# Kernel tuning notes

Measured on AMD Instinct MI355X. Metric: run time of the kernel, lower is better.

The kernel has to match this reference:

```python
import jax, jax.numpy as jnp
import numpy as np

INF = 1e10
B, T, D, N, H = 4, 1024, 1024, 16, 4096
SCALE = float(np.sqrt(D))  # Attention built with d_key = d_model in original code


def _linear(x, w, b):
    return x @ w.T + b


def _layernorm(x, gamma, beta, eps=1e-6):
    # torch x.std(-1) is unbiased (ddof=1); eps added to std, matching original
    m = x.mean(-1, keepdims=True)
    var = ((x - m) ** 2).sum(-1, keepdims=True) / (x.shape[-1] - 1)
    return gamma * (x - m) / (jnp.sqrt(var) + eps) + beta


def _mha(q_in, k_in, v_in, wq, bq, wk, bk, wv, bv, wo, bo, mask, causal):
    Bb, Tq, Dm = q_in.shape
    Tk = k_in.shape[1]
    dh = Dm // N
    q = _linear(q_in, wq, bq).reshape(Bb, Tq, N, dh).transpose(0, 2, 1, 3)  # b n q d
    k = _linear(k_in, wk, bk).reshape(Bb, Tk, N, dh).transpose(0, 2, 1, 3)
    v = _linear(v_in, wv, bv).reshape(Bb, Tk, N, dh).transpose(0, 2, 1, 3)
    dots = jnp.einsum('bnqd,bnkd->bnqk', q, k)
    if causal and Tq == Tk:
        tri = jnp.triu(jnp.ones((Tq, Tk), dots.dtype), 1) * INF
        dots = dots - tri
    dots = dots - (1.0 - mask)[:, None, None, :] * INF  # mask: 1=keep
    probs = jax.nn.softmax(dots / SCALE, axis=-1)
    out = jnp.einsum('bnqk,bnkd->bnqd', probs, v)
    out = out.transpose(0, 2, 1, 3).reshape(Bb, Tq, Dm)
    return _linear(out, wo, bo)


def setup_inputs() -> dict:
    key = jax.random.key(0)
    ks = jax.random.split(key, 16)
    g = lambda k, shp: (jax.random.normal(k, shp, dtype=jnp.float32) * 0.02)
    inp = {
        'x': jax.random.normal(ks[0], (B, T, D), dtype=jnp.float32),
        'encoding': jax.random.normal(ks[1], (B, T, D), dtype=jnp.float32),
        'mask_src': jnp.ones((B, T), dtype=jnp.float32),
        'mask_trg': jnp.ones((B, T), dtype=jnp.float32),
        # causal self-attention projections
        'sa_wq': g(ks[2], (D, D)), 'sa_bq': jnp.zeros((D,), jnp.float32),
        'sa_wk': g(ks[3], (D, D)), 'sa_bk': jnp.zeros((D,), jnp.float32),
        'sa_wv': g(ks[4], (D, D)), 'sa_bv': jnp.zeros((D,), jnp.float32),
        'sa_wo': g(ks[5], (D, D)), 'sa_bo': jnp.zeros((D,), jnp.float32),
        'sa_gamma': jnp.ones((D,), jnp.float32), 'sa_beta': jnp.zeros((D,), jnp.float32),
        # cross-attention projections
        'ca_wq': g(ks[6], (D, D)), 'ca_bq': jnp.zeros((D,), jnp.float32),
        'ca_wk': g(ks[7], (D, D)), 'ca_bk': jnp.zeros((D,), jnp.float32),
        'ca_wv': g(ks[8], (D, D)), 'ca_bv': jnp.zeros((D,), jnp.float32),
        'ca_wo': g(ks[9], (D, D)), 'ca_bo': jnp.zeros((D,), jnp.float32),
        'ca_gamma': jnp.ones((D,), jnp.float32), 'ca_beta': jnp.zeros((D,), jnp.float32),
        # feedforward
        'ff_w1': g(ks[10], (H, D)), 'ff_b1': jnp.zeros((H,), jnp.float32),
        'ff_w2': g(ks[11], (D, H)), 'ff_b2': jnp.zeros((D,), jnp.float32),
        'ff_gamma': jnp.ones((D,), jnp.float32), 'ff_beta': jnp.zeros((D,), jnp.float32),
    }
    return inp


def reference(x, encoding, mask_src, mask_trg,
              sa_wq, sa_bq, sa_wk, sa_bk, sa_wv, sa_bv, sa_wo, sa_bo, sa_gamma, sa_beta,
              ca_wq, ca_bq, ca_wk, ca_bk, ca_wv, ca_bv, ca_wo, ca_bo, ca_gamma, ca_beta,
              ff_w1, ff_b1, ff_w2, ff_b2, ff_gamma, ff_beta):
    # DecoderLayer forward (eval: dropout = identity)
    h = _layernorm(x + _mha(x, x, x, sa_wq, sa_bq, sa_wk, sa_bk, sa_wv, sa_bv,
                            sa_wo, sa_bo, mask_trg, causal=True), sa_gamma, sa_beta)
    h = _layernorm(h + _mha(h, encoding, encoding, ca_wq, ca_bq, ca_wk, ca_bk,
                            ca_wv, ca_bv, ca_wo, ca_bo, mask_src, causal=False),
                   ca_gamma, ca_beta)
    ff = _linear(jax.nn.relu(_linear(h, ff_w1, ff_b1)), ff_w2, ff_b2)
    return _layernorm(h + ff, ff_gamma, ff_beta)
```

## Files before the change

kernel.cpp:

```cpp
#include <hip/hip_runtime.h>
#include <hip/hip_bf16.h>
#include <math.h>
#include <stdint.h>

#define BATCH   4
#define TSEQ    1024
#define DMODEL  1024
#define NHEAD   16
#define DHEAD   64
#define HFF     4096
#define MROWS   (BATCH * TSEQ)

typedef _Float16 f16;
typedef __attribute__((ext_vector_type(2))) _Float16 f16x2;
typedef __attribute__((ext_vector_type(4))) _Float16 f16x4;
typedef __attribute__((ext_vector_type(8))) _Float16 f16x8;
typedef __attribute__((ext_vector_type(4))) float    f32x4;

__global__ __launch_bounds__(256)
void cvt_f32_f16(const float* __restrict__ in, f16* __restrict__ out, int n)
{
    const int i = (blockIdx.x * 256 + threadIdx.x) * 8;
    if (i < n) {
        const float4 a = *(const float4*)(in + i);
        const float4 b = *(const float4*)(in + i + 4);
        f16x8 o;
        o[0] = (_Float16)a.x; o[1] = (_Float16)a.y; o[2] = (_Float16)a.z; o[3] = (_Float16)a.w;
        o[4] = (_Float16)b.x; o[5] = (_Float16)b.y; o[6] = (_Float16)b.z; o[7] = (_Float16)b.w;
        *(f16x8*)(out + i) = o;
    }
}

template<int TN, bool RES, bool RELU>
__global__ __launch_bounds__(256, 2)
void hgemm(const f16* __restrict__ A, const f16* __restrict__ Wt,
           const float* __restrict__ bias, const f16* __restrict__ Rm,
           f16* __restrict__ C, int M, int N, int K)
{
    constexpr int TM = 128, TK = 32;
    constexpr int NB = TN / 32;
    constexpr int AISS = (TM * TK) / (256 * 8);
    constexpr int BISS = (TN * TK) / (256 * 8);
    __shared__ alignas(16) f16 As[2][TM * TK];
    __shared__ alignas(16) f16 Bs[2][TN * TK];

    const int t = threadIdx.x, ln = t & 63, wv = t >> 6;
    const int wr = wv >> 1, wc = wv & 1;
    const size_t m0 = (size_t)blockIdx.y * TM, n0 = (size_t)blockIdx.x * TN;

    f32x4 acc[4][NB];
#pragma unroll
    for (int i = 0; i < 4; ++i)
#pragma unroll
        for (int j = 0; j < NB; ++j) acc[i][j] = (f32x4){0.f, 0.f, 0.f, 0.f};

    const f16* Ag = A + (m0 + (t >> 2)) * (size_t)K + (t & 3) * 8;
    const f16* Bg = Wt + (n0 + (t >> 2)) * (size_t)K + (t & 3) * 8;

    auto stage = [&](int buf, int k0) {
#pragma unroll
        for (int i = 0; i < AISS; ++i)
            __builtin_amdgcn_global_load_lds(
                (const __attribute__((address_space(1))) unsigned int*)(Ag + (size_t)(i * 64) * K + k0),
                (__attribute__((address_space(3))) unsigned int*)(&As[buf][(i * 256 + wv * 64) * 8]),
                16, 0, 0);
#pragma unroll
        for (int i = 0; i < BISS; ++i)
            __builtin_amdgcn_global_load_lds(
                (const __attribute__((address_space(1))) unsigned int*)(Bg + (size_t)(i * 64) * K + k0),
                (__attribute__((address_space(3))) unsigned int*)(&Bs[buf][(i * 256 + wv * 64) * 8]),
                16, 0, 0);
    };

    stage(0, 0);
    __syncthreads();
    int buf = 0;
    for (int k0 = 0; k0 < K; k0 += TK) {
        if (k0 + TK < K) stage(buf ^ 1, k0 + TK);
        f16x8 af[4], bf[NB];
        const f16* Ab = As[buf];
        const f16* Bb = Bs[buf];
#pragma unroll
        for (int i = 0; i < 4; ++i)
            af[i] = *(const f16x8*)(Ab + (wr * 64 + i * 16 + (ln & 15)) * TK + (ln >> 4) * 8);
#pragma unroll
        for (int j = 0; j < NB; ++j)
            bf[j] = *(const f16x8*)(Bb + (wc * (TN / 2) + j * 16 + (ln & 15)) * TK + (ln >> 4) * 8);
#pragma unroll
        for (int i = 0; i < 4; ++i)
#pragma unroll
            for (int j = 0; j < NB; ++j)
                acc[i][j] = __builtin_amdgcn_mfma_f32_16x16x32_f16(af[i], bf[j], acc[i][j], 0, 0, 0);
        __syncthreads();
        buf ^= 1;
    }

    const int colbase = (int)n0 + wc * (TN / 2) + (ln & 15);
    const int rowbase = (int)m0 + wr * 64 + (ln >> 4) * 4;
#pragma unroll
    for (int i = 0; i < 4; ++i) {
#pragma unroll
        for (int j = 0; j < NB; ++j) {
            const int col = colbase + j * 16;
            const float bj = bias[col];
#pragma unroll
            for (int r = 0; r < 4; ++r) {
                const int row = rowbase + i * 16 + r;
                float v = acc[i][j][r] + bj;
                if (RES) v += (float)Rm[(size_t)row * N + col];
                if (RELU) v = fmaxf(v, 0.f);
                C[(size_t)row * N + col] = (f16)v;
            }
        }
    }
}

template<bool CAUSAL>
__global__ __launch_bounds__(256, 2)
void attn_mfma(const f16* __restrict__ Qp, int qstr,
               const f16* __restrict__ Kp, int kstr,
               const f16* __restrict__ Vp, int vstr,
               const float* __restrict__ maskp,
               f16* __restrict__ Op)
{
    __shared__ alignas(16) f16 Ks[64 * 64];
    __shared__ alignas(16) f16 Vt[64 * 64];
    __shared__ alignas(16) f16 Ps[4][16 * 64];
    __shared__ alignas(16) float Msk[64];

    const int t = threadIdx.x, l = t & 63, wv = t >> 6;
    const int g = l >> 4, lq = l & 15, a = l & 7;
    const int bh = blockIdx.y, b = bh >> 4, h = bh & 15;
    const int q0 = blockIdx.x * 64;
    const int q0w = q0 + wv * 16;
    const int bT = b * TSEQ;

    f16x8 qf[2];
    {
        const f16* qp = Qp + (size_t)(bT + q0w + lq) * qstr + h * 64 + g * 8;
        qf[0] = *(const f16x8*)(qp);
        qf[1] = *(const f16x8*)(qp + 32);
    }

    f32x4 oacc[4];
#pragma unroll
    for (int i = 0; i < 4; ++i) oacc[i] = (f32x4){0.f, 0.f, 0.f, 0.f};
    float mrun = -1e30f, lrun = 0.f;

    const float* mrow = maskp + b * TSEQ;
    const int kend = CAUSAL ? (q0 + 64) : TSEQ;
    const int qmaxw = q0w + 15;

    f16x8 kr0, kr1, vr0, vr1;
    float mreg = 0.f;
    const int kkey = t >> 3, kd8 = t & 7;

    auto issue_loads = [&](int k0) {
        kr0 = *(const f16x8*)(Kp + (size_t)(bT + k0 + kkey) * kstr + h * 64 + kd8 * 8);
        kr1 = *(const f16x8*)(Kp + (size_t)(bT + k0 + 32 + kkey) * kstr + h * 64 + kd8 * 8);
        vr0 = *(const f16x8*)(Vp + (size_t)(bT + k0 + l) * vstr + h * 64 + wv * 8);
        vr1 = *(const f16x8*)(Vp + (size_t)(bT + k0 + l) * vstr + h * 64 + (4 + wv) * 8);
        if (t < 64) mreg = mrow[k0 + t];
    };
    auto write_stage = [&]() {
        *(f16x8*)&Ks[kkey * 64 + ((kd8 * 8) ^ ((kkey & 7) * 8))] = kr0;
        const int k2 = kkey + 32;
        *(f16x8*)&Ks[k2 * 64 + ((kd8 * 8) ^ ((k2 & 7) * 8))] = kr1;
#pragma unroll
        for (int e = 0; e < 8; ++e) {
            const int d0 = wv * 8 + e;
            const int d1 = (4 + wv) * 8 + e;
            Vt[d0 * 64 + (l ^ (e * 8))] = vr0[e];
            Vt[d1 * 64 + (l ^ (e * 8))] = vr1[e];
        }
        if (t < 64) Msk[t] = mreg;
    };

    issue_loads(0);
    write_stage();
    __syncthreads();

    f16* Pw = Ps[wv];

    for (int k0 = 0; k0 < kend; k0 += 64) {
        const int knext = k0 + 64;
        if (knext < kend) issue_loads(knext);

        if (!CAUSAL || k0 <= qmaxw) {
            f32x4 sacc[4];
#pragma unroll
            for (int kt = 0; kt < 4; ++kt) {
                const int row = kt * 16 + lq;
                const int sw = (row & 7) * 8;
                const f16x8 a0 = *(const f16x8*)&Ks[row * 64 + ((g * 8) ^ sw)];
                const f16x8 a1 = *(const f16x8*)&Ks[row * 64 + (((4 + g) * 8) ^ sw)];
                f32x4 z = (f32x4){0.f, 0.f, 0.f, 0.f};
                z = __builtin_amdgcn_mfma_f32_16x16x32_f16(a0, qf[0], z, 0, 0, 0);
                sacc[kt] = __builtin_amdgcn_mfma_f32_16x16x32_f16(a1, qf[1], z, 0, 0, 0);
            }
            float p[4][4];
            float tmax = -3.0e38f;
#pragma unroll
            for (int kt = 0; kt < 4; ++kt) {
                const float4 mk = *(const float4*)&Msk[kt * 16 + g * 4];
                const float mka[4] = {mk.x, mk.y, mk.z, mk.w};
#pragma unroll
                for (int r = 0; r < 4; ++r) {
                    float s = sacc[kt][r] * (1.f / 32.f) - (1.f - mka[r]) * 3.125e8f;
                    if (CAUSAL) {
                        const int key = k0 + kt * 16 + g * 4 + r;
                        if (key > q0w + lq) s = -3.0e38f;
                    }
                    p[kt][r] = s;
                    tmax = fmaxf(tmax, s);
                }
            }
            tmax = fmaxf(tmax, __shfl_xor(tmax, 16));
            tmax = fmaxf(tmax, __shfl_xor(tmax, 32));
            const float mnew = fmaxf(mrun, tmax);
            const float corr = __expf(mrun - mnew);
            mrun = mnew;
            lrun *= corr;
#pragma unroll
            for (int i = 0; i < 4; ++i) {
                oacc[i][0] *= corr; oacc[i][1] *= corr;
                oacc[i][2] *= corr; oacc[i][3] *= corr;
            }
            float rsum = 0.f;
#pragma unroll
            for (int kt = 0; kt < 4; ++kt)
#pragma unroll
                for (int r = 0; r < 4; ++r) {
                    const float e = __expf(p[kt][r] - mnew);
                    p[kt][r] = e;
                    rsum += e;
                }
            rsum += __shfl_xor(rsum, 16);
            rsum += __shfl_xor(rsum, 32);
            lrun += rsum;
#pragma unroll
            for (int kt = 0; kt < 4; ++kt) {
                f16x4 pv;
                pv[0] = (_Float16)p[kt][0]; pv[1] = (_Float16)p[kt][1];
                pv[2] = (_Float16)p[kt][2]; pv[3] = (_Float16)p[kt][3];
                const int kb = kt * 16 + g * 4;
                *(f16x4*)&Pw[lq * 64 + (kb ^ (a * 8))] = pv;
            }
            const f16x8 pf0 = *(const f16x8*)&Pw[lq * 64 + ((g * 8) ^ (a * 8))];
            const f16x8 pf1 = *(const f16x8*)&Pw[lq * 64 + (((4 + g) * 8) ^ (a * 8))];
#pragma unroll
            for (int dt = 0; dt < 4; ++dt) {
                const int row = dt * 16 + lq;
                const int sw = (row & 7) * 8;
                const f16x8 v0 = *(const f16x8*)&Vt[row * 64 + ((g * 8) ^ sw)];
                const f16x8 v1 = *(const f16x8*)&Vt[row * 64 + (((4 + g) * 8) ^ sw)];
                oacc[dt] = __builtin_amdgcn_mfma_f32_16x16x32_f16(v0, pf0, oacc[dt], 0, 0, 0);
                oacc[dt] = __builtin_amdgcn_mfma_f32_16x16x32_f16(v1, pf1, oacc[dt], 0, 0, 0);
            }
        }

        __syncthreads();
        if (knext < kend) write_stage();
        __syncthreads();
    }

    const float inv = 1.f / lrun;
#pragma unroll
    for (int dt = 0; dt < 4; ++dt) {
        f16x4 ov;
        ov[0] = (_Float16)(oacc[dt][0] * inv); ov[1] = (_Float16)(oacc[dt][1] * inv);
        ov[2] = (_Float16)(oacc[dt][2] * inv); ov[3] = (_Float16)(oacc[dt][3] * inv);
        const int db = dt * 16 + g * 4;
        *(f16x4*)&Pw[lq * 64 + (db ^ (a * 8))] = ov;
    }
#pragma unroll
    for (int i = 0; i < 2; ++i) {
        const int c = i * 64 + l;
        const int row = c >> 3, c8 = c & 7;
        const f16x8 ov = *(const f16x8*)&Pw[row * 64 + ((c8 * 8) ^ ((row & 7) * 8))];
        *(f16x8*)(Op + (size_t)(bT + q0w + row) * DMODEL + h * 64 + c8 * 8) = ov;
    }
}

__inline__ __device__ float block_sum256(float v, float* sm)
{
#pragma unroll
    for (int off = 32; off > 0; off >>= 1) v += __shfl_down(v, off, 64);
    const int lane = threadIdx.x & 63, w = threadIdx.x >> 6;
    if (lane == 0) sm[w] = v;
    __syncthreads();
    const float r = sm[0] + sm[1] + sm[2] + sm[3];
    __syncthreads();
    return r;
}

template<bool F32OUT>
__global__ __launch_bounds__(256)
void ln_kernel(const f16* __restrict__ X, const float* __restrict__ g,
               const float* __restrict__ be, void* __restrict__ Yv)
{
    __shared__ float sm[4];
    const int row = blockIdx.x;
    const size_t base = (size_t)row * DMODEL + threadIdx.x * 4;
    const f16x4 xv = *(const f16x4*)(X + base);
    float x[4] = {(float)xv[0], (float)xv[1], (float)xv[2], (float)xv[3]};

    float s = x[0] + x[1] + x[2] + x[3];
    s = block_sum256(s, sm);
    const float mean = s * (1.0f / (float)DMODEL);

    float dx[4] = {x[0] - mean, x[1] - mean, x[2] - mean, x[3] - mean};
    float s2 = dx[0] * dx[0] + dx[1] * dx[1] + dx[2] * dx[2] + dx[3] * dx[3];
    s2 = block_sum256(s2, sm);
    const float rs = 1.0f / (sqrtf(s2 * (1.0f / (float)(DMODEL - 1))) + 1e-6f);

    const float4 gv = *(const float4*)(g + threadIdx.x * 4);
    const float4 bv = *(const float4*)(be + threadIdx.x * 4);
    const float y0 = gv.x * dx[0] * rs + bv.x;
    const float y1 = gv.y * dx[1] * rs + bv.y;
    const float y2 = gv.z * dx[2] * rs + bv.z;
    const float y3 = gv.w * dx[3] * rs + bv.w;
    if (F32OUT) {
        float4 y = {y0, y1, y2, y3};
        *(float4*)((float*)Yv + base) = y;
    } else {
        f16x4 y; y[0] = (_Float16)y0; y[1] = (_Float16)y1; y[2] = (_Float16)y2; y[3] = (_Float16)y3;
        *(f16x4*)((f16*)Yv + base) = y;
    }
}

extern "C" void kernel_launch(void* const* d_in, const int* in_sizes, int n_in,
                              void* d_out, int out_size, void* d_ws, size_t ws_size,
                              hipStream_t stream)
{
    (void)in_sizes; (void)n_in; (void)out_size; (void)ws_size;

    const float* x        = (const float*)d_in[0];
    const float* enc      = (const float*)d_in[1];
    const float* mask_src = (const float*)d_in[2];
    const float* mask_trg = (const float*)d_in[3];
    const float* sa_wq = (const float*)d_in[4];  const float* sa_bq = (const float*)d_in[5];
    const float* sa_wk = (const float*)d_in[6];  const float* sa_bk = (const float*)d_in[7];
    const float* sa_wv = (const float*)d_in[8];  const float* sa_bv = (const float*)d_in[9];
    const float* sa_wo = (const float*)d_in[10]; const float* sa_bo = (const float*)d_in[11];
    const float* sa_g  = (const float*)d_in[12]; const float* sa_b  = (const float*)d_in[13];
    const float* ca_wq = (const float*)d_in[14]; const float* ca_bq = (const float*)d_in[15];
    const float* ca_wk = (const float*)d_in[16]; const float* ca_bk = (const float*)d_in[17];
    const float* ca_wv = (const float*)d_in[18]; const float* ca_bv = (const float*)d_in[19];
    const float* ca_wo = (const float*)d_in[20]; const float* ca_bo = (const float*)d_in[21];
    const float* ca_g  = (const float*)d_in[22]; const float* ca_b  = (const float*)d_in[23];
    const float* ff_w1 = (const float*)d_in[24]; const float* ff_b1 = (const float*)d_in[25];
    const float* ff_w2 = (const float*)d_in[26]; const float* ff_b2 = (const float*)d_in[27];
    const float* ff_g  = (const float*)d_in[28]; const float* ff_b  = (const float*)d_in[29];

    f16* ws = (f16*)d_ws;
    const size_t MEG = 1024 * 1024;
    f16* Wh = ws;
    f16* G  = ws + 4 * MEG;
    f16* S0 = ws + 20 * MEG;
    f16* S1 = ws + 24 * MEG;
    f16* S2 = ws + 28 * MEG;
    f16* S3 = ws + 32 * MEG;
    f16* S4 = ws + 36 * MEG;
    f16* S5 = ws + 40 * MEG;
    float* Bias = (float*)((char*)d_ws + 88 * MEG);

    const int NACT = MROWS * DMODEL;
    const int NW   = DMODEL * DMODEL;

    dim3 blk(256);
    const int cvAct = NACT / 2048, cvW = NW / 2048, cvFF = (4 * NW) / 2048;
    dim3 gQKV(3072 / 128, MROWS / 128);
    dim3 gN64(DMODEL / 64, MROWS / 128);
    dim3 gKV(2048 / 128, MROWS / 128);
    dim3 gFF1(HFF / 128, MROWS / 128);
    dim3 agrid(TSEQ / 64, BATCH * NHEAD);

    cvt_f32_f16<<<cvAct, blk, 0, stream>>>(x, S0, NACT);
    cvt_f32_f16<<<cvAct, blk, 0, stream>>>(enc, S1, NACT);
    cvt_f32_f16<<<cvW, blk, 0, stream>>>(sa_wq, Wh, NW);
    cvt_f32_f16<<<cvW, blk, 0, stream>>>(sa_wk, Wh + 1 * MEG, NW);
    cvt_f32_f16<<<cvW, blk, 0, stream>>>(sa_wv, Wh + 2 * MEG, NW);
    hipMemcpyAsync(Bias + 0,    sa_bq, 4096, hipMemcpyDeviceToDevice, stream);
    hipMemcpyAsync(Bias + 1024, sa_bk, 4096, hipMemcpyDeviceToDevice, stream);
    hipMemcpyAsync(Bias + 2048, sa_bv, 4096, hipMemcpyDeviceToDevice, stream);
    hgemm<128, false, false><<<gQKV, blk, 0, stream>>>(S0, Wh, Bias, nullptr, G, MROWS, 3072, DMODEL);
    attn_mfma<true><<<agrid, blk, 0, stream>>>(G, 3072, G + 1024, 3072, G + 2048, 3072, mask_trg, S2);
    cvt_f32_f16<<<cvW, blk, 0, stream>>>(sa_wo, Wh, NW);
    hipMemcpyAsync(Bias, sa_bo, 4096, hipMemcpyDeviceToDevice, stream);
    hgemm<64, true, false><<<gN64, blk, 0, stream>>>(S2, Wh, Bias, S0, S3, MROWS, DMODEL, DMODEL);
    ln_kernel<false><<<MROWS, blk, 0, stream>>>(S3, sa_g, sa_b, S4);

    cvt_f32_f16<<<cvW, blk, 0, stream>>>(ca_wq, Wh, NW);
    hipMemcpyAsync(Bias, ca_bq, 4096, hipMemcpyDeviceToDevice, stream);
    hgemm<64, false, false><<<gN64, blk, 0, stream>>>(S4, Wh, Bias, nullptr, G, MROWS, DMODEL, DMODEL);
    cvt_f32_f16<<<cvW, blk, 0, stream>>>(ca_wk, Wh, NW);
    cvt_f32_f16<<<cvW, blk, 0, stream>>>(ca_wv, Wh + 1 * MEG, NW);
    hipMemcpyAsync(Bias + 0,    ca_bk, 4096, hipMemcpyDeviceToDevice, stream);
    hipMemcpyAsync(Bias + 1024, ca_bv, 4096, hipMemcpyDeviceToDevice, stream);
    hgemm<128, false, false><<<gKV, blk, 0, stream>>>(S1, Wh, Bias, nullptr, G + 4 * MEG, MROWS, 2048, DMODEL);
    attn_mfma<false><<<agrid, blk, 0, stream>>>(G, 1024, G + 4 * MEG, 2048, G + 4 * MEG + 1024, 2048, mask_src, S2);
    cvt_f32_f16<<<cvW, blk, 0, stream>>>(ca_wo, Wh, NW);
    hipMemcpyAsync(Bias, ca_bo, 4096, hipMemcpyDeviceToDevice, stream);
    hgemm<64, true, false><<<gN64, blk, 0, stream>>>(S2, Wh, Bias, S4, S3, MROWS, DMODEL, DMODEL);
    ln_kernel<false><<<MROWS, blk, 0, stream>>>(S3, ca_g, ca_b, S5);

    cvt_f32_f16<<<cvFF, blk, 0, stream>>>(ff_w1, Wh, 4 * NW);
    hipMemcpyAsync(Bias, ff_b1, 16384, hipMemcpyDeviceToDevice, stream);
    hgemm<128, false, true><<<gFF1, blk, 0, stream>>>(S5, Wh, Bias, nullptr, G, MROWS, HFF, DMODEL);
    cvt_f32_f16<<<cvFF, blk, 0, stream>>>(ff_w2, Wh, 4 * NW);
    hipMemcpyAsync(Bias, ff_b2, 4096, hipMemcpyDeviceToDevice, stream);
    hgemm<64, true, false><<<gN64, blk, 0, stream>>>(G, Wh, Bias, S5, S3, MROWS, DMODEL, HFF);
    ln_kernel<true><<<MROWS, blk, 0, stream>>>(S3, ff_g, ff_b, d_out);
}
```

Before: 574.4 us.

## Fuse fp32 weight conversion into GEMM B-loads and swizzle block order

The GEMM now reads fp32 weights straight from the original buffers, converts them to fp16 in registers and writes them to LDS. This removes the separate weight-conversion kernels and the bias memcpys, and bias is indexed per 1024-column segment. It also fixes the N tile at 128 for every GEMM and adds an 8-way block-index swizzle meant to improve cache locality. In exchange, each GEMM reads twice the weight bytes per tile, the B path goes through registers instead of the direct global-to-LDS load, and the N=1024 GEMMs launch fewer blocks.

```diff
diff --git a/kernel.cpp b/kernel.cpp
--- a/kernel.cpp
+++ b/kernel.cpp
@@ -31,22 +31,37 @@
     }
 }
 
-template<int TN, bool RES, bool RELU>
+template<bool RES, bool RELU>
 __global__ __launch_bounds__(256, 2)
-void hgemm(const f16* __restrict__ A, const f16* __restrict__ Wt,
-           const float* __restrict__ bias, const f16* __restrict__ Rm,
-           f16* __restrict__ C, int M, int N, int K)
-{
-    constexpr int TM = 128, TK = 32;
-    constexpr int NB = TN / 32;
-    constexpr int AISS = (TM * TK) / (256 * 8);
-    constexpr int BISS = (TN * TK) / (256 * 8);
+void hgemm(const f16* __restrict__ A,
+           const float* __restrict__ w0, const float* __restrict__ w1,
+           const float* __restrict__ w2, const float* __restrict__ w3,
+           const float* __restrict__ b0, const float* __restrict__ b1,
+           const float* __restrict__ b2, const float* __restrict__ b3,
+           const f16* __restrict__ Rm, f16* __restrict__ C,
+           int M, int N, int K)
+{
+    constexpr int TM = 128, TN = 128, TK = 32;
+    constexpr int NB = 4;
+    constexpr int AISS = 2;
+    constexpr int BISS = 2;
     __shared__ alignas(16) f16 As[2][TM * TK];
     __shared__ alignas(16) f16 Bs[2][TN * TK];
 
     const int t = threadIdx.x, ln = t & 63, wv = t >> 6;
     const int wr = wv >> 1, wc = wv & 1;
-    const size_t m0 = (size_t)blockIdx.y * TM, n0 = (size_t)blockIdx.x * TN;
+
+    const int gx = gridDim.x, nb = gx * gridDim.y;
+    const int d  = blockIdx.y * gx + blockIdx.x;
+    const int wid = (d & 7) * (nb >> 3) + (d >> 3);
+    const int bx = wid % gx, by = wid / gx;
+
+    const size_t m0 = (size_t)by * TM, n0 = (size_t)bx * TN;
+
+    const float* wseg[4] = {w0, w1, w2, w3};
+    const float* bseg[4] = {b0, b1, b2, b3};
+    const float* Wg = wseg[n0 >> 10] + ((n0 & 1023) + (t >> 2)) * (size_t)K + (t & 3) * 8;
+    const f16*   Ag = A + (m0 + (t >> 2)) * (size_t)K + (t & 3) * 8;
 
     f32x4 acc[4][NB];
 #pragma unroll
@@ -54,29 +69,45 @@
 #pragma unroll
         for (int j = 0; j < NB; ++j) acc[i][j] = (f32x4){0.f, 0.f, 0.f, 0.f};
 
-    const f16* Ag = A + (m0 + (t >> 2)) * (size_t)K + (t & 3) * 8;
-    const f16* Bg = Wt + (n0 + (t >> 2)) * (size_t)K + (t & 3) * 8;
-
-    auto stage = [&](int buf, int k0) {
+    auto stage_A = [&](int buf, int k0) {
 #pragma unroll
         for (int i = 0; i < AISS; ++i)
             __builtin_amdgcn_global_load_lds(
                 (const __attribute__((address_space(1))) unsigned int*)(Ag + (size_t)(i * 64) * K + k0),
                 (__attribute__((address_space(3))) unsigned int*)(&As[buf][(i * 256 + wv * 64) * 8]),
                 16, 0, 0);
-#pragma unroll
-        for (int i = 0; i < BISS; ++i)
-            __builtin_amdgcn_global_load_lds(
-                (const __attribute__((address_space(1))) unsigned int*)(Bg + (size_t)(i * 64) * K + k0),
-                (__attribute__((address_space(3))) unsigned int*)(&Bs[buf][(i * 256 + wv * 64) * 8]),
-                16, 0, 0);
     };
 
-    stage(0, 0);
+    float4 br[BISS][2];
+    auto issue_B = [&](int k0) {
+#pragma unroll
+        for (int i = 0; i < BISS; ++i) {
+            br[i][0] = *(const float4*)(Wg + (size_t)(i * 64) * K + k0);
+            br[i][1] = *(const float4*)(Wg + (size_t)(i * 64) * K + k0 + 4);
+        }
+    };
+    auto write_B = [&](int buf) {
+#pragma unroll
+        for (int i = 0; i < BISS; ++i) {
+            f16x8 v;
+            v[0] = (_Float16)br[i][0].x; v[1] = (_Float16)br[i][0].y;
+            v[2] = (_Float16)br[i][0].z; v[3] = (_Float16)br[i][0].w;
+            v[4] = (_Float16)br[i][1].x; v[5] = (_Float16)br[i][1].y;
+            v[6] = (_Float16)br[i][1].z; v[7] = (_Float16)br[i][1].w;
+            *(f16x8*)&Bs[buf][(i * 256 + t) * 8] = v;
+        }
+    };
+
+    stage_A(0, 0);
+    issue_B(0);
+    write_B(0);
     __syncthreads();
+
     int buf = 0;
     for (int k0 = 0; k0 < K; k0 += TK) {
-        if (k0 + TK < K) stage(buf ^ 1, k0 + TK);
+        const int knext = k0 + TK;
+        if (knext < K) { stage_A(buf ^ 1, knext); issue_B(knext); }
+
         f16x8 af[4], bf[NB];
         const f16* Ab = As[buf];
         const f16* Bb = Bs[buf];
@@ -85,24 +116,26 @@
             af[i] = *(const f16x8*)(Ab + (wr * 64 + i * 16 + (ln & 15)) * TK + (ln >> 4) * 8);
 #pragma unroll
         for (int j = 0; j < NB; ++j)
-            bf[j] = *(const f16x8*)(Bb + (wc * (TN / 2) + j * 16 + (ln & 15)) * TK + (ln >> 4) * 8);
+            bf[j] = *(const f16x8*)(Bb + (wc * 64 + j * 16 + (ln & 15)) * TK + (ln >> 4) * 8);
 #pragma unroll
         for (int i = 0; i < 4; ++i)
 #pragma unroll
             for (int j = 0; j < NB; ++j)
                 acc[i][j] = __builtin_amdgcn_mfma_f32_16x16x32_f16(af[i], bf[j], acc[i][j], 0, 0, 0);
+
+        if (knext < K) write_B(buf ^ 1);
         __syncthreads();
         buf ^= 1;
     }
 
-    const int colbase = (int)n0 + wc * (TN / 2) + (ln & 15);
+    const int colbase = (int)n0 + wc * 64 + (ln & 15);
     const int rowbase = (int)m0 + wr * 64 + (ln >> 4) * 4;
 #pragma unroll
     for (int i = 0; i < 4; ++i) {
 #pragma unroll
         for (int j = 0; j < NB; ++j) {
             const int col = colbase + j * 16;
-            const float bj = bias[col];
+            const float bj = bseg[col >> 10][col & 1023];
 #pragma unroll
             for (int r = 0; r < 4; ++r) {
                 const int row = rowbase + i * 16 + r;
@@ -355,7 +388,6 @@
 
     f16* ws = (f16*)d_ws;
     const size_t MEG = 1024 * 1024;
-    f16* Wh = ws;
     f16* G  = ws + 4 * MEG;
     f16* S0 = ws + 20 * MEG;
     f16* S1 = ws + 24 * MEG;
@@ -363,53 +395,46 @@
     f16* S3 = ws + 32 * MEG;
     f16* S4 = ws + 36 * MEG;
     f16* S5 = ws + 40 * MEG;
-    float* Bias = (float*)((char*)d_ws + 88 * MEG);
 
     const int NACT = MROWS * DMODEL;
-    const int NW   = DMODEL * DMODEL;
 
     dim3 blk(256);
-    const int cvAct = NACT / 2048, cvW = NW / 2048, cvFF = (4 * NW) / 2048;
+    const int cvAct = NACT / 2048;
     dim3 gQKV(3072 / 128, MROWS / 128);
-    dim3 gN64(DMODEL / 64, MROWS / 128);
-    dim3 gKV(2048 / 128, MROWS / 128);
-    dim3 gFF1(HFF / 128, MROWS / 128);
+    dim3 gN1 (1024 / 128, MROWS / 128);
+    dim3 gKV (2048 / 128, MROWS / 128);
+    dim3 gFF1(4096 / 128, MROWS / 128);
     dim3 agrid(TSEQ / 64, BATCH * NHEAD);
 
     cvt_f32_f16<<<cvAct, blk, 0, stream>>>(x, S0, NACT);
     cvt_f32_f16<<<cvAct, blk, 0, stream>>>(enc, S1, NACT);
-    cvt_f32_f16<<<cvW, blk, 0, stream>>>(sa_wq, Wh, NW);
-    cvt_f32_f16<<<cvW, blk, 0, stream>>>(sa_wk, Wh + 1 * MEG, NW);
-    cvt_f32_f16<<<cvW, blk, 0, stream>>>(sa_wv, Wh + 2 * MEG, NW);
-    hipMemcpyAsync(Bias + 0,    sa_bq, 4096, hipMemcpyDeviceToDevice, stream);
-    hipMemcpyAsync(Bias + 1024, sa_bk, 4096, hipMemcpyDeviceToDevice, stream);
-    hipMemcpyAsync(Bias + 2048, sa_bv, 4096, hipMemcpyDeviceToDevice, stream);
-    hgemm<128, false, false><<<gQKV, blk, 0, stream>>>(S0, Wh, Bias, nullptr, G, MROWS, 3072, DMODEL);
+    hgemm<false, false><<<gQKV, blk, 0, stream>>>(S0,
+        sa_wq, sa_wk, sa_wv, sa_wv, sa_bq, sa_bk, sa_bv, sa_bv,
+        nullptr, G, MROWS, 3072, DMODEL);
     attn_mfma<true><<<agrid, blk, 0, stream>>>(G, 3072, G + 1024, 3072, G + 2048, 3072, mask_trg, S2);
-    cvt_f32_f16<<<cvW, blk, 0, stream>>>(sa_wo, Wh, NW);
-    hipMemcpyAsync(Bias, sa_bo, 4096, hipMemcpyDeviceToDevice, stream);
-    hgemm<64, true, false><<<gN64, blk, 0, stream>>>(S2, Wh, Bias, S0, S3, MROWS, DMODEL, DMODEL);
+    hgemm<true, false><<<gN1, blk, 0, stream>>>(S2,
+        sa_wo, sa_wo, sa_wo, sa_wo, sa_bo, sa_bo, sa_bo, sa_bo,
+        S0, S3, MROWS, DMODEL, DMODEL);
     ln_kernel<false><<<MROWS, blk, 0, stream>>>(S3, sa_g, sa_b, S4);
 
-    cvt_f32_f16<<<cvW, blk, 0, stream>>>(ca_wq, Wh, NW);
-    hipMemcpyAsync(Bias, ca_bq, 4096, hipMemcpyDeviceToDevice, stream);
-    hgemm<64, false, false><<<gN64, blk, 0, stream>>>(S4, Wh, Bias, nullptr, G, MROWS, DMODEL, DMODEL);
-    cvt_f32_f16<<<cvW, blk, 0, stream>>>(ca_wk, Wh, NW);
-    cvt_f32_f16<<<cvW, blk, 0, stream>>>(ca_wv, Wh + 1 * MEG, NW);
-    hipMemcpyAsync(Bias + 0,    ca_bk, 4096, hipMemcpyDeviceToDevice, stream);
-    hipMemcpyAsync(Bias + 1024, ca_bv, 4096, hipMemcpyDeviceToDevice, stream);
-    hgemm<128, false, false><<<gKV, blk, 0, stream>>>(S1, Wh, Bias, nullptr, G + 4 * MEG, MROWS, 2048, DMODEL);
+    hgemm<false, false><<<gN1, blk, 0, stream>>>(S4,
+        ca_wq, ca_wq, ca_wq, ca_wq, ca_bq, ca_bq, ca_bq, ca_bq,
+        nullptr, G, MROWS, DMODEL, DMODEL);
+    hgemm<false, false><<<gKV, blk, 0, stream>>>(S1,
+        ca_wk, ca_wv, ca_wv, ca_wv, ca_bk, ca_bv, ca_bv, ca_bv,
+        nullptr, G + 4 * MEG, MROWS, 2048, DMODEL);
     attn_mfma<false><<<agrid, blk, 0, stream>>>(G, 1024, G + 4 * MEG, 2048, G + 4 * MEG + 1024, 2048, mask_src, S2);
-    cvt_f32_f16<<<cvW, blk, 0, stream>>>(ca_wo, Wh, NW);
-    hipMemcpyAsync(Bias, ca_bo, 4096, hipMemcpyDeviceToDevice, stream);
-    hgemm<64, true, false><<<gN64, blk, 0, stream>>>(S2, Wh, Bias, S4, S3, MROWS, DMODEL, DMODEL);
+    hgemm<true, false><<<gN1, blk, 0, stream>>>(S2,
+        ca_wo, ca_wo, ca_wo, ca_wo, ca_bo, ca_bo, ca_bo, ca_bo,
+        S4, S3, MROWS, DMODEL, DMODEL);
     ln_kernel<false><<<MROWS, blk, 0, stream>>>(S3, ca_g, ca_b, S5);
 
-    cvt_f32_f16<<<cvFF, blk, 0, stream>>>(ff_w1, Wh, 4 * NW);
-    hipMemcpyAsync(Bias, ff_b1, 16384, hipMemcpyDeviceToDevice, stream);
-    hgemm<128, false, true><<<gFF1, blk, 0, stream>>>(S5, Wh, Bias, nullptr, G, MROWS, HFF, DMODEL);
-    cvt_f32_f16<<<cvFF, blk, 0, stream>>>(ff_w2, Wh, 4 * NW);
-    hipMemcpyAsync(Bias, ff_b2, 4096, hipMemcpyDeviceToDevice, stream);
-    hgemm<64, true, false><<<gN64, blk, 0, stream>>>(G, Wh, Bias, S5, S3, MROWS, DMODEL, HFF);
+    hgemm<false, true><<<gFF1, blk, 0, stream>>>(S5,
+        ff_w1, ff_w1 + 1024 * (size_t)DMODEL, ff_w1 + 2048 * (size_t)DMODEL, ff_w1 + 3072 * (size_t)DMODEL,
+        ff_b1, ff_b1 + 1024, ff_b1 + 2048, ff_b1 + 3072,
+        nullptr, G, MROWS, HFF, DMODEL);
+    hgemm<true, false><<<gN1, blk, 0, stream>>>(G,
+        ff_w2, ff_w2, ff_w2, ff_w2, ff_b2, ff_b2, ff_b2, ff_b2,
+        S5, S3, MROWS, DMODEL, HFF);
     ln_kernel<true><<<MROWS, blk, 0, stream>>>(S3, ff_g, ff_b, d_out);
 }
```

New measurement: 644.8 us. 12.3% more time.
